# Kernel optimization log

Measured on AMD Instinct MI355X. Metric: run time of the kernel, lower is better.

The kernel has to match this reference:

```python
import jax, jax.numpy as jnp
import numpy as np

WS = (2, 7, 7)          # window size (Wd, Wh, Ww)
SS = (1, 3, 3)          # shift size
DIM = 96
HEADS = 3
HD = DIM // HEADS       # head dim = 32
N = WS[0] * WS[1] * WS[2]  # 98 tokens per window
EPS = 1e-5


def _rel_index():
    c = np.stack(np.meshgrid(np.arange(WS[0]), np.arange(WS[1]), np.arange(WS[2]), indexing='ij')).reshape(3, -1)
    r = (c[:, :, None] - c[:, None, :]).transpose(1, 2, 0)  # (N, N, 3)
    r[..., 0] += WS[0] - 1
    r[..., 1] += WS[1] - 1
    r[..., 2] += WS[2] - 1
    r[..., 0] *= (2 * WS[1] - 1) * (2 * WS[2] - 1)
    r[..., 1] *= 2 * WS[2] - 1
    return jnp.asarray(r.sum(-1))  # (N, N) int

REL_IDX = _rel_index()


def _ln(x, w, b):
    m = x.mean(-1, keepdims=True)
    v = ((x - m) ** 2).mean(-1, keepdims=True)
    return (x - m) * jax.lax.rsqrt(v + EPS) * w + b


def setup_inputs() -> dict:
    key = jax.random.key(0)
    ks = jax.random.split(key, 10)
    B, D, H, W, C = 2, 16, 112, 112, DIM
    nW = (D // WS[0]) * (H // WS[1]) * (W // WS[2])  # 2048
    s = 0.02
    tbl = (2 * WS[0] - 1) * (2 * WS[1] - 1) * (2 * WS[2] - 1)
    return dict(
        x=jax.random.normal(ks[0], (B, D, H, W, C), jnp.float32),
        mask=jax.random.normal(ks[1], (nW, N, N), jnp.float32),
        norm1_w=jnp.ones((C,), jnp.float32), norm1_b=jnp.zeros((C,), jnp.float32),
        qkv_w=jax.random.normal(ks[2], (C, 3 * C), jnp.float32) * s,
        qkv_b=jnp.zeros((3 * C,), jnp.float32),
        rpb_table=jax.random.normal(ks[3], (tbl, HEADS), jnp.float32) * s,
        proj_w=jax.random.normal(ks[4], (C, C), jnp.float32) * s,
        proj_b=jnp.zeros((C,), jnp.float32),
        norm2_w=jnp.ones((C,), jnp.float32), norm2_b=jnp.zeros((C,), jnp.float32),
        fc1_w=jax.random.normal(ks[5], (C, 4 * C), jnp.float32) * s,
        fc1_b=jnp.zeros((4 * C,), jnp.float32),
        fc2_w=jax.random.normal(ks[6], (4 * C, C), jnp.float32) * s,
        fc2_b=jnp.zeros((C,), jnp.float32),
    )


def reference(x, mask, norm1_w, norm1_b, qkv_w, qkv_b, rpb_table, proj_w, proj_b,
              norm2_w, norm2_b, fc1_w, fc1_b, fc2_w, fc2_b):
    B, D, H, W, C = x.shape
    shortcut = x
    x = _ln(x, norm1_w, norm1_b)
    # shift (dims divisible by window -> no padding needed)
    x = jnp.roll(x, shift=(-SS[0], -SS[1], -SS[2]), axis=(1, 2, 3))
    nd, nh, nw = D // WS[0], H // WS[1], W // WS[2]
    # window partition -> (B*nW, N, C)
    xw = x.reshape(B, nd, WS[0], nh, WS[1], nw, WS[2], C)
    xw = xw.transpose(0, 1, 3, 5, 2, 4, 6, 7).reshape(-1, N, C)
    B_ = xw.shape[0]
    qkv = (xw @ qkv_w + qkv_b).reshape(B_, N, 3, HEADS, HD).transpose(2, 0, 3, 1, 4)
    q, k, v = qkv[0] * (HD ** -0.5), qkv[1], qkv[2]
    attn = jnp.einsum('bhnd,bhmd->bhnm', q, k)  # (B_, H, N, N)
    bias = rpb_table[REL_IDX.reshape(-1)].reshape(N, N, HEADS).transpose(2, 0, 1)
    attn = attn + bias[None]
    nWm = mask.shape[0]
    attn = attn.reshape(B_ // nWm, nWm, HEADS, N, N) + mask[None, :, None]
    attn = jax.nn.softmax(attn.reshape(B_, HEADS, N, N), axis=-1)
    out = jnp.einsum('bhnm,bhmd->bhnd', attn, v).transpose(0, 2, 1, 3).reshape(B_, N, C)
    out = out @ proj_w + proj_b
    # window reverse
    x = out.reshape(B, nd, nh, nw, WS[0], WS[1], WS[2], C)
    x = x.transpose(0, 1, 4, 2, 5, 3, 6, 7).reshape(B, D, H, W, C)
    x = jnp.roll(x, shift=SS, axis=(1, 2, 3))
    x = shortcut + x
    y = _ln(x, norm2_w, norm2_b)
    y = jax.nn.gelu(y @ fc1_w + fc1_b, approximate=False) @ fc2_w + fc2_b
    return x + y
```

## Files before the change

kernel.cpp:

```cpp
#include <hip/hip_runtime.h>

typedef float f32x4 __attribute__((ext_vector_type(4)));
typedef __bf16 bf16x8 __attribute__((ext_vector_type(8)));
typedef unsigned short ushort_t;
typedef ushort_t us4 __attribute__((ext_vector_type(4)));
typedef ushort_t us8 __attribute__((ext_vector_type(8)));
typedef unsigned int u32x4 __attribute__((ext_vector_type(4)));

#define MFMA16(a, b, c) __builtin_amdgcn_mfma_f32_16x16x32_bf16((a), (b), (c), 0, 0, 0)

__device__ __forceinline__ ushort_t f2bf(float f) {
    unsigned int u = __builtin_bit_cast(unsigned int, f);
    u += 0x7fffu + ((u >> 16) & 1u);
    return (ushort_t)(u >> 16);
}

__device__ __forceinline__ unsigned int packbf2(float lo, float hi) {
    return ((unsigned int)f2bf(hi) << 16) | (unsigned int)f2bf(lo);
}

__device__ __forceinline__ float gelu_fast(float x) {
    float x2 = x * x;
    float t = __builtin_fmaf(0.044715f * x2, x, x);
    float e = __builtin_amdgcn_exp2f(t * (-1.5957691216f * 1.44269504f));
    return x * __builtin_amdgcn_rcpf(1.0f + e);
}

#define NTOK 98
#define CCH 96
#define QSCALE 0.17677669529663687f

#define WQKVP_OFF   ((size_t)0)
#define WPROJP_OFF  (WQKVP_OFF + (size_t)27648 * 2)
#define WFC1P_OFF   (WPROJP_OFF + (size_t)9216 * 2)
#define WFC2P_OFF   (WFC1P_OFF + (size_t)36864 * 2)
#define BIAS_OFF    (WFC2P_OFF + (size_t)36864 * 2)

__global__ __launch_bounds__(256) void prep_kernel(
    const float* __restrict__ qkv_w, const float* __restrict__ proj_w,
    const float* __restrict__ fc1_w, const float* __restrict__ fc2_w,
    const float* __restrict__ rpb,
    ushort_t* __restrict__ wqkvP, ushort_t* __restrict__ wprojP,
    ushort_t* __restrict__ wfc1P, ushort_t* __restrict__ wfc2P,
    float* __restrict__ bias)
{
    int i = blockIdx.x * 256 + threadIdx.x;
    if (i < 27648) {
        int f = i >> 9, r = i & 511, lane = r >> 3, m = r & 7;
        int k0 = f % 3, t = f / 3, nt = t % 2, t2 = t / 2, w = t2 % 3, h = t2 / 3;
        int row = k0 * 32 + (lane >> 4) * 8 + m;
        int col = w * 96 + h * 32 + nt * 16 + (lane & 15);
        wqkvP[i] = f2bf(qkv_w[row * 288 + col]);
        return;
    }
    i -= 27648;
    if (i < 9216) {
        int f = i >> 9, r = i & 511, lane = r >> 3, m = r & 7;
        int k0 = f % 3, nt = f / 3;
        int row = k0 * 32 + (lane >> 4) * 8 + m;
        int col = nt * 16 + (lane & 15);
        wprojP[i] = f2bf(proj_w[row * 96 + col]);
        return;
    }
    i -= 9216;
    if (i < 36864) {
        int f = i >> 9, r = i & 511, lane = r >> 3, m = r & 7;
        int k0 = f % 3, nt = f / 3;
        int row = k0 * 32 + (lane >> 4) * 8 + m;
        int col = nt * 16 + (lane & 15);
        wfc1P[i] = f2bf(fc1_w[row * 384 + col]);
        return;
    }
    i -= 36864;
    if (i < 36864) {
        int f = i >> 9, r = i & 511, lane = r >> 3, m = r & 7;
        int k0 = f % 12, nt = f / 12;
        int row = k0 * 32 + (lane >> 4) * 8 + m;
        int col = nt * 16 + (lane & 15);
        wfc2P[i] = f2bf(fc2_w[row * 96 + col]);
        return;
    }
    i -= 36864;
    if (i < 28812) {
        int h = i / 9604, rem = i % 9604, r = rem / 98, c = rem % 98;
        int rd = r / 49 - c / 49 + 1;
        int rh = (r % 49) / 7 - (c % 49) / 7 + 6;
        int rw = r % 7 - c % 7 + 6;
        int idx = (rd * 13 + rh) * 13 + rw;
        bias[i] = rpb[idx * 3 + h];
    }
}

__global__ __launch_bounds__(192, 3) void fused_attn(
    const float* __restrict__ x, const float* __restrict__ mask,
    const float* __restrict__ n1w, const float* __restrict__ n1b,
    const float* __restrict__ qkv_b, const float* __restrict__ proj_b,
    const ushort_t* __restrict__ wqkvP, const ushort_t* __restrict__ wprojP,
    const float* __restrict__ bias, float* __restrict__ dout)
{
    __shared__ ushort_t xw_lds[112 * 104];
    __shared__ ushort_t sc_all[3][2176];
    __shared__ int tokbase[112];

    const int tid  = threadIdx.x;
    const int lane = tid & 63;
    const int wave = tid >> 6;
    const int l16  = lane & 15, lg = lane >> 4;

    const int b  = blockIdx.x;
    const int wm = (b & 7) * 256 + ((b >> 3) >> 1);
    const int bb = (b >> 3) & 1;
    const int id_ = wm >> 8, ih = (wm >> 4) & 15, iw = wm & 15;

    if (tid < 98) {
        int td = tid / 49, r49 = tid - td * 49, th = r49 / 7, tw = r49 - th * 7;
        int od = (id_ * 2 + td + 1) & 15;
        int oh = ih * 7 + th + 3; if (oh >= 112) oh -= 112;
        int ow = iw * 7 + tw + 3; if (ow >= 112) ow -= 112;
        tokbase[tid] = ((((bb << 4) + od) * 112 + oh) * 112 + ow) * 96;
    }
    {
        us4 z4 = {0, 0, 0, 0};
        for (int i = tid; i < 14 * 26; i += 192) {
            int t = 98 + i / 26, c4 = (i % 26) * 4;
            *(us4*)(xw_lds + t * 104 + c4) = z4;
        }
    }
    __syncthreads();

    {
        const int g = tid >> 5, lane32 = tid & 31;
        for (int t = g; t < 98; t += 6) {
            const float* xp = x + tokbase[t];
            float v0 = xp[lane32], v1 = xp[lane32 + 32], v2 = xp[lane32 + 64];
            float s = v0 + v1 + v2, sq = v0 * v0 + v1 * v1 + v2 * v2;
            #pragma unroll
            for (int m = 1; m < 32; m <<= 1) { s += __shfl_xor(s, m); sq += __shfl_xor(sq, m); }
            float mean = s * (1.0f / 96.0f);
            float var = sq * (1.0f / 96.0f) - mean * mean;
            float rs = rsqrtf(var + 1e-5f);
            ushort_t* op = xw_lds + t * 104;
            op[lane32]      = f2bf((v0 - mean) * rs * n1w[lane32]      + n1b[lane32]);
            op[lane32 + 32] = f2bf((v1 - mean) * rs * n1w[lane32 + 32] + n1b[lane32 + 32]);
            op[lane32 + 64] = f2bf((v2 - mean) * rs * n1w[lane32 + 64] + n1b[lane32 + 64]);
        }
    }
    __syncthreads();

    const int h = wave;
    ushort_t* sc = sc_all[wave];
    const float* biash = bias + h * 9604;
    const float* maskw = mask + (size_t)wm * 9604;

    bf16x8 qf[7], kf[7], vf[2][4];

    #pragma unroll
    for (int which = 0; which < 2; ++which) {
        bf16x8 bw[2][3];
        float  bia[2];
        #pragma unroll
        for (int nt = 0; nt < 2; ++nt) {
            bia[nt] = qkv_b[which * 96 + h * 32 + nt * 16 + l16];
            #pragma unroll
            for (int k0 = 0; k0 < 3; ++k0)
                bw[nt][k0] = *(const bf16x8*)(wqkvP + ((((h * 3 + which) * 2 + nt) * 3 + k0) << 9) + lane * 8);
        }
        for (int mt = 0; mt < 7; ++mt) {
            const ushort_t* ap = xw_lds + (mt * 16 + l16) * 104 + lg * 8;
            bf16x8 a0 = *(const bf16x8*)(ap);
            bf16x8 a1 = *(const bf16x8*)(ap + 32);
            bf16x8 a2 = *(const bf16x8*)(ap + 64);
            #pragma unroll
            for (int nt = 0; nt < 2; ++nt) {
                f32x4 acc = {0.f, 0.f, 0.f, 0.f};
                acc = MFMA16(a0, bw[nt][0], acc);
                acc = MFMA16(a1, bw[nt][1], acc);
                acc = MFMA16(a2, bw[nt][2], acc);
                float scl = (which == 0) ? QSCALE : 1.0f;
                #pragma unroll
                for (int j = 0; j < 4; ++j)
                    sc[(lg * 4 + j) * 36 + nt * 16 + l16] = f2bf((acc[j] + bia[nt]) * scl);
            }
            if (which == 0) qf[mt] = *(const bf16x8*)(sc + l16 * 36 + lg * 8);
            else            kf[mt] = *(const bf16x8*)(sc + l16 * 36 + lg * 8);
        }
    }

    {
        bf16x8 bw[2][3];
        float  bia[2];
        #pragma unroll
        for (int nt = 0; nt < 2; ++nt) {
            bia[nt] = qkv_b[192 + h * 32 + nt * 16 + l16];
            #pragma unroll
            for (int k0 = 0; k0 < 3; ++k0)
                bw[nt][k0] = *(const bf16x8*)(wqkvP + ((((h * 3 + 2) * 2 + nt) * 3 + k0) << 9) + lane * 8);
        }
        #pragma unroll
        for (int k0 = 0; k0 < 4; ++k0) {
            unsigned int pk[2][2][2];
            #pragma unroll
            for (int half = 0; half < 2; ++half) {
                int mtp = 2 * k0 + half;
                if (mtp < 7) {
                    const ushort_t* ap = xw_lds + (mtp * 16 + l16) * 104 + lg * 8;
                    bf16x8 a0 = *(const bf16x8*)(ap);
                    bf16x8 a1 = *(const bf16x8*)(ap + 32);
                    bf16x8 a2 = *(const bf16x8*)(ap + 64);
                    #pragma unroll
                    for (int nt2 = 0; nt2 < 2; ++nt2) {
                        f32x4 acc = {0.f, 0.f, 0.f, 0.f};
                        acc = MFMA16(a0, bw[nt2][0], acc);
                        acc = MFMA16(a1, bw[nt2][1], acc);
                        acc = MFMA16(a2, bw[nt2][2], acc);
                        pk[half][nt2][0] = packbf2(acc[0] + bia[nt2], acc[1] + bia[nt2]);
                        pk[half][nt2][1] = packbf2(acc[2] + bia[nt2], acc[3] + bia[nt2]);
                    }
                } else {
                    pk[half][0][0] = pk[half][0][1] = 0u;
                    pk[half][1][0] = pk[half][1][1] = 0u;
                }
            }
            #pragma unroll
            for (int nt2 = 0; nt2 < 2; ++nt2) {
                u32x4 w;
                #pragma unroll
                for (int e = 0; e < 4; ++e) {
                    int s = l16 + 16 * (2 * (lg & 1) + (e >> 1));
                    unsigned int t0 = (unsigned int)__shfl((int)pk[0][nt2][e & 1], s, 64);
                    unsigned int t1 = (unsigned int)__shfl((int)pk[1][nt2][e & 1], s, 64);
                    w[e] = (lg >> 1) ? t1 : t0;
                }
                vf[nt2][k0] = __builtin_bit_cast(bf16x8, w);
            }
        }
    }
    __syncthreads();

    ushort_t* out = xw_lds;

    if (lane < 32) {
        us8 z = {0, 0, 0, 0, 0, 0, 0, 0};
        *(us8*)(sc + (lane >> 1) * 136 + 112 + (lane & 1) * 8) = z;
    }

    #pragma unroll
    for (int mt = 0; mt < 7; ++mt) {
        f32x4 sv[7];
        #pragma unroll
        for (int nt = 0; nt < 7; ++nt) {
            f32x4 z = {0.f, 0.f, 0.f, 0.f};
            sv[nt] = MFMA16(qf[mt], kf[nt], z);
        }
        const int r0 = mt * 16 + lg * 4;
        const bool ctail = (l16 < 2);
        #pragma unroll
        for (int j = 0; j < 4; ++j) {
            int r = r0 + j;
            if (r < 98) {
                const float* bp_ = biash + r * 98;
                const float* mp_ = maskw + r * 98;
                #pragma unroll
                for (int nt = 0; nt < 6; ++nt) {
                    int c = nt * 16 + l16;
                    sv[nt][j] += bp_[c] + mp_[c];
                }
                if (ctail) sv[6][j] += bp_[96 + l16] + mp_[96 + l16];
                else       sv[6][j] = -1e30f;
            } else {
                #pragma unroll
                for (int nt = 0; nt < 7; ++nt) sv[nt][j] = -1e30f;
            }
        }
        f32x4 inv;
        #pragma unroll
        for (int j = 0; j < 4; ++j) {
            float sum = 0.f;
            #pragma unroll
            for (int nt = 0; nt < 7; ++nt) { float e = __expf(sv[nt][j]); sv[nt][j] = e; sum += e; }
            sum += __shfl_xor(sum, 1); sum += __shfl_xor(sum, 2);
            sum += __shfl_xor(sum, 4); sum += __shfl_xor(sum, 8);
            inv[j] = __builtin_amdgcn_rcpf(sum);
        }
        #pragma unroll
        for (int j = 0; j < 4; ++j)
            #pragma unroll
            for (int nt = 0; nt < 7; ++nt)
                sc[(lg * 4 + j) * 136 + nt * 16 + l16] = f2bf(sv[nt][j]);
        bf16x8 pf[4];
        #pragma unroll
        for (int k0 = 0; k0 < 4; ++k0)
            pf[k0] = *(const bf16x8*)(sc + l16 * 136 + k0 * 32 + lg * 8);
        #pragma unroll
        for (int nt2 = 0; nt2 < 2; ++nt2) {
            f32x4 acc = {0.f, 0.f, 0.f, 0.f};
            #pragma unroll
            for (int k0 = 0; k0 < 4; ++k0) acc = MFMA16(pf[k0], vf[nt2][k0], acc);
            #pragma unroll
            for (int j = 0; j < 4; ++j) {
                int tok = mt * 16 + lg * 4 + j;
                if (tok < 98)
                    out[tok * 104 + h * 32 + nt2 * 16 + l16] = f2bf(acc[j] * inv[j]);
            }
        }
    }
    __syncthreads();

    for (int job = wave; job < 42; job += 3) {
        int mt = job / 6, nt = job % 6;
        int cg = nt * 16 + l16;
        f32x4 acc = {0.f, 0.f, 0.f, 0.f};
        #pragma unroll
        for (int k0 = 0; k0 < 3; ++k0) {
            bf16x8 ao = *(const bf16x8*)(out + (mt * 16 + l16) * 104 + k0 * 32 + lg * 8);
            bf16x8 bp = *(const bf16x8*)(wprojP + ((nt * 3 + k0) << 9) + lane * 8);
            acc = MFMA16(ao, bp, acc);
        }
        float pb = proj_b[cg];
        #pragma unroll
        for (int j = 0; j < 4; ++j) {
            int tok = mt * 16 + lg * 4 + j;
            if (tok < 98) {
                int g = tokbase[tok] + cg;
                dout[g] = x[g] + acc[j] + pb;
            }
        }
    }
}

__global__ __launch_bounds__(512, 2) void mlp_kernel(
    float* __restrict__ xres, const float* __restrict__ w2, const float* __restrict__ b2,
    const ushort_t* __restrict__ wfc1P, const float* __restrict__ fc1_b,
    const ushort_t* __restrict__ wfc2P, const float* __restrict__ fc2_b)
{
    __shared__ ushort_t A_ln[64 * 104];
    __shared__ ushort_t h_lds[64 * 392];
    const int tid = threadIdx.x;
    const int lane = tid & 63, wave = tid >> 6;
    const int l16 = lane & 15, lg = lane >> 4;
    const size_t t0 = (size_t)blockIdx.x * 64;

    {
        int t = tid >> 3, sub = tid & 7;
        const float* xp = xres + (t0 + t) * 96;
        f32x4 v[3];
        float s = 0.f, sq = 0.f;
        #pragma unroll
        for (int j4 = 0; j4 < 3; ++j4) {
            v[j4] = *(const f32x4*)(xp + (j4 * 8 + sub) * 4);
            #pragma unroll
            for (int e = 0; e < 4; ++e) { s += v[j4][e]; sq += v[j4][e] * v[j4][e]; }
        }
        s += __shfl_xor(s, 1); s += __shfl_xor(s, 2); s += __shfl_xor(s, 4);
        sq += __shfl_xor(sq, 1); sq += __shfl_xor(sq, 2); sq += __shfl_xor(sq, 4);
        float mean = s * (1.0f / 96.0f);
        float var = sq * (1.0f / 96.0f) - mean * mean;
        float rs = rsqrtf(var + 1e-5f);
        #pragma unroll
        for (int j4 = 0; j4 < 3; ++j4) {
            int c0 = (j4 * 8 + sub) * 4;
            us4 pk;
            #pragma unroll
            for (int e = 0; e < 4; ++e)
                pk[e] = f2bf((v[j4][e] - mean) * rs * w2[c0 + e] + b2[c0 + e]);
            *(us4*)(A_ln + t * 104 + c0) = pk;
        }
    }
    __syncthreads();

    for (int job = wave; job < 96; job += 8) {
        int mt = job / 24, nt = job % 24;
        int n = nt * 16 + l16;
        f32x4 acc = {0.f, 0.f, 0.f, 0.f};
        #pragma unroll
        for (int k0 = 0; k0 < 3; ++k0) {
            bf16x8 a  = *(const bf16x8*)(A_ln + (mt * 16 + l16) * 104 + k0 * 32 + lg * 8);
            bf16x8 bw = *(const bf16x8*)(wfc1P + ((nt * 3 + k0) << 9) + lane * 8);
            acc = MFMA16(a, bw, acc);
        }
        float bv = fc1_b[n];
        #pragma unroll
        for (int j = 0; j < 4; ++j) {
            int tok = mt * 16 + lg * 4 + j;
            h_lds[tok * 392 + n] = f2bf(gelu_fast(acc[j] + bv));
        }
    }
    __syncthreads();

    for (int job = wave; job < 24; job += 8) {
        int mt = job / 6, nt = job % 6;
        int c = nt * 16 + l16;
        f32x4 acc = {0.f, 0.f, 0.f, 0.f};
        #pragma unroll
        for (int k0 = 0; k0 < 12; ++k0) {
            bf16x8 a  = *(const bf16x8*)(h_lds + (mt * 16 + l16) * 392 + k0 * 32 + lg * 8);
            bf16x8 bw = *(const bf16x8*)(wfc2P + ((nt * 12 + k0) << 9) + lane * 8);
            acc = MFMA16(a, bw, acc);
        }
        float bv = fc2_b[c];
        #pragma unroll
        for (int j = 0; j < 4; ++j) {
            int tok = mt * 16 + lg * 4 + j;
            size_t g = (t0 + tok) * 96 + c;
            xres[g] = xres[g] + acc[j] + bv;
        }
    }
}

extern "C" void kernel_launch(void* const* d_in, const int* in_sizes, int n_in,
                              void* d_out, int out_size, void* d_ws, size_t ws_size,
                              hipStream_t stream) {
    const float* x      = (const float*)d_in[0];
    const float* mask   = (const float*)d_in[1];
    const float* n1w    = (const float*)d_in[2];
    const float* n1b    = (const float*)d_in[3];
    const float* qkv_w  = (const float*)d_in[4];
    const float* qkv_b  = (const float*)d_in[5];
    const float* rpb    = (const float*)d_in[6];
    const float* proj_w = (const float*)d_in[7];
    const float* proj_b = (const float*)d_in[8];
    const float* n2w    = (const float*)d_in[9];
    const float* n2b    = (const float*)d_in[10];
    const float* fc1_w  = (const float*)d_in[11];
    const float* fc1_b  = (const float*)d_in[12];
    const float* fc2_w  = (const float*)d_in[13];
    const float* fc2_b  = (const float*)d_in[14];

    char* ws = (char*)d_ws;
    ushort_t* wqkvP  = (ushort_t*)(ws + WQKVP_OFF);
    ushort_t* wprojP = (ushort_t*)(ws + WPROJP_OFF);
    ushort_t* wfc1P  = (ushort_t*)(ws + WFC1P_OFF);
    ushort_t* wfc2P  = (ushort_t*)(ws + WFC2P_OFF);
    float*    biasp  = (float*)(ws + BIAS_OFF);
    float*    dout   = (float*)d_out;

    prep_kernel<<<545, 256, 0, stream>>>(qkv_w, proj_w, fc1_w, fc2_w, rpb,
                                         wqkvP, wprojP, wfc1P, wfc2P, biasp);
    fused_attn<<<4096, 192, 0, stream>>>(x, mask, n1w, n1b, qkv_b, proj_b,
                                         wqkvP, wprojP, biasp, dout);
    mlp_kernel<<<6272, 512, 0, stream>>>(dout, n2w, n2b, wfc1P, fc1_b, wfc2P, fc2_b);
}
```

Baseline: 571.8 us.

## Transpose score tile and keep softmax in registers with bf16 mask/bias

Computes S^T (keys x queries) with MFMA so each lane's softmax reduction runs across lane groups, and builds the P operand for P·V through lane shuffles instead of an LDS round trip. The mask and relative-position bias are pre-transposed and converted to bf16 by a new pre-pass kernel, which halves their bytes read per window. The smaller LDS footprint lets occupancy rise to 4 blocks per SIMD. The cost is an extra kernel that reads the whole fp32 mask and writes a bf16 copy every call, plus a small loss of precision in the mask and bias.

```diff
diff --git a/kernel.cpp b/kernel.cpp
--- a/kernel.cpp
+++ b/kernel.cpp
@@ -4,7 +4,6 @@
 typedef __bf16 bf16x8 __attribute__((ext_vector_type(8)));
 typedef unsigned short ushort_t;
 typedef ushort_t us4 __attribute__((ext_vector_type(4)));
-typedef ushort_t us8 __attribute__((ext_vector_type(8)));
 typedef unsigned int u32x4 __attribute__((ext_vector_type(4)));
 
 #define MFMA16(a, b, c) __builtin_amdgcn_mfma_f32_16x16x32_bf16((a), (b), (c), 0, 0, 0)
@@ -14,7 +13,9 @@
     u += 0x7fffu + ((u >> 16) & 1u);
     return (ushort_t)(u >> 16);
 }
-
+__device__ __forceinline__ float bf2f(ushort_t u) {
+    return __builtin_bit_cast(float, (unsigned int)u << 16);
+}
 __device__ __forceinline__ unsigned int packbf2(float lo, float hi) {
     return ((unsigned int)f2bf(hi) << 16) | (unsigned int)f2bf(lo);
 }
@@ -34,7 +35,8 @@
 #define WPROJP_OFF  (WQKVP_OFF + (size_t)27648 * 2)
 #define WFC1P_OFF   (WPROJP_OFF + (size_t)9216 * 2)
 #define WFC2P_OFF   (WFC1P_OFF + (size_t)36864 * 2)
-#define BIAS_OFF    (WFC2P_OFF + (size_t)36864 * 2)
+#define BIAST_OFF   (WFC2P_OFF + (size_t)36864 * 2)
+#define MASKT_OFF   (BIAST_OFF + (size_t)28812 * 2 + 4096)
 
 __global__ __launch_bounds__(256) void prep_kernel(
     const float* __restrict__ qkv_w, const float* __restrict__ proj_w,
@@ -42,7 +44,7 @@
     const float* __restrict__ rpb,
     ushort_t* __restrict__ wqkvP, ushort_t* __restrict__ wprojP,
     ushort_t* __restrict__ wfc1P, ushort_t* __restrict__ wfc2P,
-    float* __restrict__ bias)
+    ushort_t* __restrict__ biasT)
 {
     int i = blockIdx.x * 256 + threadIdx.x;
     if (i < 27648) {
@@ -82,24 +84,39 @@
     }
     i -= 36864;
     if (i < 28812) {
-        int h = i / 9604, rem = i % 9604, r = rem / 98, c = rem % 98;
-        int rd = r / 49 - c / 49 + 1;
-        int rh = (r % 49) / 7 - (c % 49) / 7 + 6;
-        int rw = r % 7 - c % 7 + 6;
+        int h = i / 9604, rem = i % 9604, kc = rem / 98, qr = rem % 98;
+        int rd = qr / 49 - kc / 49 + 1;
+        int rh = (qr % 49) / 7 - (kc % 49) / 7 + 6;
+        int rw = qr % 7 - kc % 7 + 6;
         int idx = (rd * 13 + rh) * 13 + rw;
-        bias[i] = rpb[idx * 3 + h];
-    }
-}
-
-__global__ __launch_bounds__(192, 3) void fused_attn(
-    const float* __restrict__ x, const float* __restrict__ mask,
+        biasT[i] = f2bf(rpb[idx * 3 + h]);
+    }
+}
+
+__global__ __launch_bounds__(256) void maskT_kernel(
+    const float* __restrict__ mask, ushort_t* __restrict__ maskT)
+{
+    __shared__ float m_lds[9604];
+    const int wm = blockIdx.x;
+    const float* mw = mask + (size_t)wm * 9604;
+    for (int i = threadIdx.x; i < 9604; i += 256) m_lds[i] = mw[i];
+    __syncthreads();
+    ushort_t* out = maskT + (size_t)wm * 9604;
+    for (int i = threadIdx.x; i < 9604; i += 256) {
+        int kc = i / 98, qr = i - kc * 98;
+        out[i] = f2bf(m_lds[qr * 98 + kc]);
+    }
+}
+
+__global__ __launch_bounds__(192, 4) void fused_attn(
+    const float* __restrict__ x, const ushort_t* __restrict__ maskT,
     const float* __restrict__ n1w, const float* __restrict__ n1b,
     const float* __restrict__ qkv_b, const float* __restrict__ proj_b,
     const ushort_t* __restrict__ wqkvP, const ushort_t* __restrict__ wprojP,
-    const float* __restrict__ bias, float* __restrict__ dout)
+    const ushort_t* __restrict__ biasT, float* __restrict__ dout)
 {
     __shared__ ushort_t xw_lds[112 * 104];
-    __shared__ ushort_t sc_all[3][2176];
+    __shared__ ushort_t sc_all[3][576];
     __shared__ int tokbase[112];
 
     const int tid  = threadIdx.x;
@@ -149,8 +166,8 @@
 
     const int h = wave;
     ushort_t* sc = sc_all[wave];
-    const float* biash = bias + h * 9604;
-    const float* maskw = mask + (size_t)wm * 9604;
+    const ushort_t* bTh = biasT + h * 9604;
+    const ushort_t* mTw = maskT + (size_t)wm * 9604;
 
     bf16x8 qf[7], kf[7], vf[2][4];
 
@@ -198,7 +215,7 @@
         }
         #pragma unroll
         for (int k0 = 0; k0 < 4; ++k0) {
-            unsigned int pk[2][2][2];
+            unsigned int pkv[2][2][2];
             #pragma unroll
             for (int half = 0; half < 2; ++half) {
                 int mtp = 2 * k0 + half;
@@ -213,12 +230,12 @@
                         acc = MFMA16(a0, bw[nt2][0], acc);
                         acc = MFMA16(a1, bw[nt2][1], acc);
                         acc = MFMA16(a2, bw[nt2][2], acc);
-                        pk[half][nt2][0] = packbf2(acc[0] + bia[nt2], acc[1] + bia[nt2]);
-                        pk[half][nt2][1] = packbf2(acc[2] + bia[nt2], acc[3] + bia[nt2]);
+                        pkv[half][nt2][0] = packbf2(acc[0] + bia[nt2], acc[1] + bia[nt2]);
+                        pkv[half][nt2][1] = packbf2(acc[2] + bia[nt2], acc[3] + bia[nt2]);
                     }
                 } else {
-                    pk[half][0][0] = pk[half][0][1] = 0u;
-                    pk[half][1][0] = pk[half][1][1] = 0u;
+                    pkv[half][0][0] = pkv[half][0][1] = 0u;
+                    pkv[half][1][0] = pkv[half][1][1] = 0u;
                 }
             }
             #pragma unroll
@@ -227,8 +244,8 @@
                 #pragma unroll
                 for (int e = 0; e < 4; ++e) {
                     int s = l16 + 16 * (2 * (lg & 1) + (e >> 1));
-                    unsigned int t0 = (unsigned int)__shfl((int)pk[0][nt2][e & 1], s, 64);
-                    unsigned int t1 = (unsigned int)__shfl((int)pk[1][nt2][e & 1], s, 64);
+                    unsigned int t0 = (unsigned int)__shfl((int)pkv[0][nt2][e & 1], s, 64);
+                    unsigned int t1 = (unsigned int)__shfl((int)pkv[1][nt2][e & 1], s, 64);
                     w[e] = (lg >> 1) ? t1 : t0;
                 }
                 vf[nt2][k0] = __builtin_bit_cast(bf16x8, w);
@@ -239,58 +256,69 @@
 
     ushort_t* out = xw_lds;
 
-    if (lane < 32) {
-        us8 z = {0, 0, 0, 0, 0, 0, 0, 0};
-        *(us8*)(sc + (lane >> 1) * 136 + 112 + (lane & 1) * 8) = z;
-    }
-
     #pragma unroll
     for (int mt = 0; mt < 7; ++mt) {
-        f32x4 sv[7];
+        const int qr = mt * 16 + l16;
+        const ushort_t* mTl = mTw + (lg * 4) * 98 + qr;
+        const ushort_t* bTl = bTh + (lg * 4) * 98 + qr;
+
+        float sum = 0.f;
+        unsigned int pk0[7], pk1[7];
         #pragma unroll
         for (int nt = 0; nt < 7; ++nt) {
             f32x4 z = {0.f, 0.f, 0.f, 0.f};
-            sv[nt] = MFMA16(qf[mt], kf[nt], z);
-        }
-        const int r0 = mt * 16 + lg * 4;
-        const bool ctail = (l16 < 2);
-        #pragma unroll
-        for (int j = 0; j < 4; ++j) {
-            int r = r0 + j;
-            if (r < 98) {
-                const float* bp_ = biash + r * 98;
-                const float* mp_ = maskw + r * 98;
-                #pragma unroll
-                for (int nt = 0; nt < 6; ++nt) {
-                    int c = nt * 16 + l16;
-                    sv[nt][j] += bp_[c] + mp_[c];
+            f32x4 stv = MFMA16(kf[nt], qf[mt], z);
+            float e0, e1, e2, e3;
+            float ev[4];
+            #pragma unroll
+            for (int j = 0; j < 4; ++j) {
+                float val;
+                if (nt < 6) {
+                    val = stv[j] + bf2f(mTl[(nt * 16 + j) * 98]) + bf2f(bTl[(nt * 16 + j) * 98]);
+                } else {
+                    int kin = lg * 4 + j;
+                    if (kin < 2)
+                        val = stv[j] + bf2f(mTl[(96 + j) * 98]) + bf2f(bTl[(96 + j) * 98]);
+                    else
+                        val = -1e30f;
                 }
-                if (ctail) sv[6][j] += bp_[96 + l16] + mp_[96 + l16];
-                else       sv[6][j] = -1e30f;
-            } else {
-                #pragma unroll
-                for (int nt = 0; nt < 7; ++nt) sv[nt][j] = -1e30f;
-            }
-        }
-        f32x4 inv;
-        #pragma unroll
-        for (int j = 0; j < 4; ++j) {
-            float sum = 0.f;
-            #pragma unroll
-            for (int nt = 0; nt < 7; ++nt) { float e = __expf(sv[nt][j]); sv[nt][j] = e; sum += e; }
-            sum += __shfl_xor(sum, 1); sum += __shfl_xor(sum, 2);
-            sum += __shfl_xor(sum, 4); sum += __shfl_xor(sum, 8);
-            inv[j] = __builtin_amdgcn_rcpf(sum);
-        }
-        #pragma unroll
-        for (int j = 0; j < 4; ++j)
-            #pragma unroll
-            for (int nt = 0; nt < 7; ++nt)
-                sc[(lg * 4 + j) * 136 + nt * 16 + l16] = f2bf(sv[nt][j]);
+                float e_ = __expf(val);
+                sum += e_;
+                ev[j] = e_;
+            }
+            e0 = ev[0]; e1 = ev[1]; e2 = ev[2]; e3 = ev[3];
+            pk0[nt] = packbf2(e0, e1);
+            pk1[nt] = packbf2(e2, e3);
+        }
+        sum += __shfl_xor(sum, 16);
+        sum += __shfl_xor(sum, 32);
+        float inv = __builtin_amdgcn_rcpf(sum);
+
         bf16x8 pf[4];
         #pragma unroll
-        for (int k0 = 0; k0 < 4; ++k0)
-            pf[k0] = *(const bf16x8*)(sc + l16 * 136 + k0 * 32 + lg * 8);
+        for (int k0 = 0; k0 < 4; ++k0) {
+            u32x4 w;
+            #pragma unroll
+            for (int e = 0; e < 4; ++e) {
+                int s = l16 + 16 * (2 * (lg & 1) + (e >> 1));
+                unsigned int a_ = (e & 1) ? pk1[2 * k0] : pk0[2 * k0];
+                unsigned int t0 = (unsigned int)__shfl((int)a_, s, 64);
+                unsigned int t1;
+                if (k0 < 3) {
+                    unsigned int b_ = (e & 1) ? pk1[2 * k0 + 1] : pk0[2 * k0 + 1];
+                    t1 = (unsigned int)__shfl((int)b_, s, 64);
+                } else {
+                    t1 = 0u;
+                }
+                w[e] = (lg >> 1) ? t1 : t0;
+            }
+            pf[k0] = __builtin_bit_cast(bf16x8, w);
+        }
+
+        float invj[4];
+        #pragma unroll
+        for (int j = 0; j < 4; ++j) invj[j] = __shfl(inv, lg * 4 + j, 64);
+
         #pragma unroll
         for (int nt2 = 0; nt2 < 2; ++nt2) {
             f32x4 acc = {0.f, 0.f, 0.f, 0.f};
@@ -300,7 +328,7 @@
             for (int j = 0; j < 4; ++j) {
                 int tok = mt * 16 + lg * 4 + j;
                 if (tok < 98)
-                    out[tok * 104 + h * 32 + nt2 * 16 + l16] = f2bf(acc[j] * inv[j]);
+                    out[tok * 104 + h * 32 + nt2 * 16 + l16] = f2bf(acc[j] * invj[j]);
             }
         }
     }
@@ -431,12 +459,14 @@
     ushort_t* wprojP = (ushort_t*)(ws + WPROJP_OFF);
     ushort_t* wfc1P  = (ushort_t*)(ws + WFC1P_OFF);
     ushort_t* wfc2P  = (ushort_t*)(ws + WFC2P_OFF);
-    float*    biasp  = (float*)(ws + BIAS_OFF);
+    ushort_t* biasT  = (ushort_t*)(ws + BIAST_OFF);
+    ushort_t* maskT  = (ushort_t*)(ws + MASKT_OFF);
     float*    dout   = (float*)d_out;
 
     prep_kernel<<<545, 256, 0, stream>>>(qkv_w, proj_w, fc1_w, fc2_w, rpb,
-                                         wqkvP, wprojP, wfc1P, wfc2P, biasp);
-    fused_attn<<<4096, 192, 0, stream>>>(x, mask, n1w, n1b, qkv_b, proj_b,
-                                         wqkvP, wprojP, biasp, dout);
+                                         wqkvP, wprojP, wfc1P, wfc2P, biasT);
+    maskT_kernel<<<2048, 256, 0, stream>>>(mask, maskT);
+    fused_attn<<<4096, 192, 0, stream>>>(x, maskT, n1w, n1b, qkv_b, proj_b,
+                                         wqkvP, wprojP, biasT, dout);
     mlp_kernel<<<6272, 512, 0, stream>>>(dout, n2w, n2b, wfc1P, fc1_b, wfc2P, fc2_b);
 }
```

Result: slower. 667.4 us (+16.7%).

## Pre-convert mask and bias to padded bf16 MFMA layout for vectorized loads

Applied to the files above, without the earlier changes.

Adds a kernel that converts the per-window attention mask to bf16 in a tile-padded layout matching MFMA output fragments, and stores the relative position bias the same way. The attention kernel then loads mask and bias with vector loads and fuses exp and row-sum into the score loop, dropping the boundary branches. This trades scattered fp32 scalar loads for an extra conversion pass over the full mask each call and reduced mask/bias precision.

```diff
diff --git a/kernel.cpp b/kernel.cpp
--- a/kernel.cpp
+++ b/kernel.cpp
@@ -4,7 +4,6 @@
 typedef __bf16 bf16x8 __attribute__((ext_vector_type(8)));
 typedef unsigned short ushort_t;
 typedef ushort_t us4 __attribute__((ext_vector_type(4)));
-typedef ushort_t us8 __attribute__((ext_vector_type(8)));
 typedef unsigned int u32x4 __attribute__((ext_vector_type(4)));
 
 #define MFMA16(a, b, c) __builtin_amdgcn_mfma_f32_16x16x32_bf16((a), (b), (c), 0, 0, 0)
@@ -14,7 +13,9 @@
     u += 0x7fffu + ((u >> 16) & 1u);
     return (ushort_t)(u >> 16);
 }
-
+__device__ __forceinline__ float bf2f(ushort_t u) {
+    return __builtin_bit_cast(float, (unsigned int)u << 16);
+}
 __device__ __forceinline__ unsigned int packbf2(float lo, float hi) {
     return ((unsigned int)f2bf(hi) << 16) | (unsigned int)f2bf(lo);
 }
@@ -34,7 +35,8 @@
 #define WPROJP_OFF  (WQKVP_OFF + (size_t)27648 * 2)
 #define WFC1P_OFF   (WPROJP_OFF + (size_t)9216 * 2)
 #define WFC2P_OFF   (WFC1P_OFF + (size_t)36864 * 2)
-#define BIAS_OFF    (WFC2P_OFF + (size_t)36864 * 2)
+#define BIAS2_OFF   (WFC2P_OFF + (size_t)36864 * 2)
+#define MASK2_OFF   (BIAS2_OFF + (size_t)37632 * 2 + 256)
 
 __global__ __launch_bounds__(256) void prep_kernel(
     const float* __restrict__ qkv_w, const float* __restrict__ proj_w,
@@ -42,7 +44,7 @@
     const float* __restrict__ rpb,
     ushort_t* __restrict__ wqkvP, ushort_t* __restrict__ wprojP,
     ushort_t* __restrict__ wfc1P, ushort_t* __restrict__ wfc2P,
-    float* __restrict__ bias)
+    ushort_t* __restrict__ bias2)
 {
     int i = blockIdx.x * 256 + threadIdx.x;
     if (i < 27648) {
@@ -81,22 +83,49 @@
         return;
     }
     i -= 36864;
-    if (i < 28812) {
-        int h = i / 9604, rem = i % 9604, r = rem / 98, c = rem % 98;
-        int rd = r / 49 - c / 49 + 1;
-        int rh = (r % 49) / 7 - (c % 49) / 7 + 6;
-        int rw = r % 7 - c % 7 + 6;
-        int idx = (rd * 13 + rh) * 13 + rw;
-        bias[i] = rpb[idx * 3 + h];
+    if (i < 37632) {
+        int h = i / 12544, rem = i % 12544;
+        int mt = rem / 1792, rem2 = rem % 1792, kc = rem2 >> 4, r16 = rem2 & 15;
+        int row = mt * 16 + r16;
+        float v = 0.f;
+        if (row < 98 && kc < 98) {
+            int rd = row / 49 - kc / 49 + 1;
+            int rh = (row % 49) / 7 - (kc % 49) / 7 + 6;
+            int rw = row % 7 - kc % 7 + 6;
+            v = rpb[((rd * 13 + rh) * 13 + rw) * 3 + h];
+        }
+        bias2[i] = f2bf(v);
+    }
+}
+
+__global__ __launch_bounds__(256) void mask2_kernel(
+    const float* __restrict__ mask, ushort_t* __restrict__ mask2)
+{
+    __shared__ float m_lds[9604];
+    const int wm = blockIdx.x;
+    const float* mw = mask + (size_t)wm * 9604;
+    for (int i = threadIdx.x; i < 9604; i += 256) m_lds[i] = mw[i];
+    __syncthreads();
+    ushort_t* out = mask2 + (size_t)wm * 12544;
+    for (int g = threadIdx.x; g < 3136; g += 256) {
+        int mt = g / 448, rem = g % 448, kc = rem >> 2, r4 = (rem & 3) * 4;
+        us4 o;
+        #pragma unroll
+        for (int e = 0; e < 4; ++e) {
+            int row = mt * 16 + r4 + e;
+            float v = (row < 98 && kc < 98) ? m_lds[row * 98 + kc] : -1e30f;
+            o[e] = f2bf(v);
+        }
+        *(us4*)(out + (size_t)g * 4) = o;
     }
 }
 
 __global__ __launch_bounds__(192, 3) void fused_attn(
-    const float* __restrict__ x, const float* __restrict__ mask,
+    const float* __restrict__ x, const ushort_t* __restrict__ mask2,
     const float* __restrict__ n1w, const float* __restrict__ n1b,
     const float* __restrict__ qkv_b, const float* __restrict__ proj_b,
     const ushort_t* __restrict__ wqkvP, const ushort_t* __restrict__ wprojP,
-    const float* __restrict__ bias, float* __restrict__ dout)
+    const ushort_t* __restrict__ bias2, float* __restrict__ dout)
 {
     __shared__ ushort_t xw_lds[112 * 104];
     __shared__ ushort_t sc_all[3][2176];
@@ -149,8 +178,8 @@
 
     const int h = wave;
     ushort_t* sc = sc_all[wave];
-    const float* biash = bias + h * 9604;
-    const float* maskw = mask + (size_t)wm * 9604;
+    const ushort_t* m2w = mask2 + (size_t)wm * 12544;
+    const ushort_t* b2h = bias2 + (size_t)h * 12544;
 
     bf16x8 qf[7], kf[7], vf[2][4];
 
@@ -198,7 +227,7 @@
         }
         #pragma unroll
         for (int k0 = 0; k0 < 4; ++k0) {
-            unsigned int pk[2][2][2];
+            unsigned int pkv[2][2][2];
             #pragma unroll
             for (int half = 0; half < 2; ++half) {
                 int mtp = 2 * k0 + half;
@@ -213,12 +242,12 @@
                         acc = MFMA16(a0, bw[nt2][0], acc);
                         acc = MFMA16(a1, bw[nt2][1], acc);
                         acc = MFMA16(a2, bw[nt2][2], acc);
-                        pk[half][nt2][0] = packbf2(acc[0] + bia[nt2], acc[1] + bia[nt2]);
-                        pk[half][nt2][1] = packbf2(acc[2] + bia[nt2], acc[3] + bia[nt2]);
+                        pkv[half][nt2][0] = packbf2(acc[0] + bia[nt2], acc[1] + bia[nt2]);
+                        pkv[half][nt2][1] = packbf2(acc[2] + bia[nt2], acc[3] + bia[nt2]);
                     }
                 } else {
-                    pk[half][0][0] = pk[half][0][1] = 0u;
-                    pk[half][1][0] = pk[half][1][1] = 0u;
+                    pkv[half][0][0] = pkv[half][0][1] = 0u;
+                    pkv[half][1][0] = pkv[half][1][1] = 0u;
                 }
             }
             #pragma unroll
@@ -227,8 +256,8 @@
                 #pragma unroll
                 for (int e = 0; e < 4; ++e) {
                     int s = l16 + 16 * (2 * (lg & 1) + (e >> 1));
-                    unsigned int t0 = (unsigned int)__shfl((int)pk[0][nt2][e & 1], s, 64);
-                    unsigned int t1 = (unsigned int)__shfl((int)pk[1][nt2][e & 1], s, 64);
+                    unsigned int t0 = (unsigned int)__shfl((int)pkv[0][nt2][e & 1], s, 64);
+                    unsigned int t1 = (unsigned int)__shfl((int)pkv[1][nt2][e & 1], s, 64);
                     w[e] = (lg >> 1) ? t1 : t0;
                 }
                 vf[nt2][k0] = __builtin_bit_cast(bf16x8, w);
@@ -240,53 +269,41 @@
     ushort_t* out = xw_lds;
 
     if (lane < 32) {
-        us8 z = {0, 0, 0, 0, 0, 0, 0, 0};
-        *(us8*)(sc + (lane >> 1) * 136 + 112 + (lane & 1) * 8) = z;
+        us4 z4 = {0, 0, 0, 0};
+        *(us4*)(sc + (lane >> 1) * 136 + 112 + (lane & 1) * 8) = z4;
+        *(us4*)(sc + (lane >> 1) * 136 + 116 + (lane & 1) * 8) = z4;
     }
 
     #pragma unroll
     for (int mt = 0; mt < 7; ++mt) {
-        f32x4 sv[7];
+        const ushort_t* m2t = m2w + mt * 1792;
+        const ushort_t* b2t = b2h + mt * 1792;
+        us4 mv[7];
+        #pragma unroll
+        for (int nt = 0; nt < 7; ++nt)
+            mv[nt] = *(const us4*)(m2t + (nt * 16 + l16) * 16 + lg * 4);
+
+        f32x4 sums = {0.f, 0.f, 0.f, 0.f};
         #pragma unroll
         for (int nt = 0; nt < 7; ++nt) {
+            us4 bv = *(const us4*)(b2t + (nt * 16 + l16) * 16 + lg * 4);
             f32x4 z = {0.f, 0.f, 0.f, 0.f};
-            sv[nt] = MFMA16(qf[mt], kf[nt], z);
-        }
-        const int r0 = mt * 16 + lg * 4;
-        const bool ctail = (l16 < 2);
+            f32x4 stv = MFMA16(qf[mt], kf[nt], z);
+            #pragma unroll
+            for (int j = 0; j < 4; ++j) {
+                float e_ = __expf(stv[j] + bf2f(mv[nt][j]) + bf2f(bv[j]));
+                sums[j] += e_;
+                sc[(lg * 4 + j) * 136 + nt * 16 + l16] = f2bf(e_);
+            }
+        }
+        f32x4 inv;
         #pragma unroll
         for (int j = 0; j < 4; ++j) {
-            int r = r0 + j;
-            if (r < 98) {
-                const float* bp_ = biash + r * 98;
-                const float* mp_ = maskw + r * 98;
-                #pragma unroll
-                for (int nt = 0; nt < 6; ++nt) {
-                    int c = nt * 16 + l16;
-                    sv[nt][j] += bp_[c] + mp_[c];
-                }
-                if (ctail) sv[6][j] += bp_[96 + l16] + mp_[96 + l16];
-                else       sv[6][j] = -1e30f;
-            } else {
-                #pragma unroll
-                for (int nt = 0; nt < 7; ++nt) sv[nt][j] = -1e30f;
-            }
-        }
-        f32x4 inv;
-        #pragma unroll
-        for (int j = 0; j < 4; ++j) {
-            float sum = 0.f;
-            #pragma unroll
-            for (int nt = 0; nt < 7; ++nt) { float e = __expf(sv[nt][j]); sv[nt][j] = e; sum += e; }
-            sum += __shfl_xor(sum, 1); sum += __shfl_xor(sum, 2);
-            sum += __shfl_xor(sum, 4); sum += __shfl_xor(sum, 8);
-            inv[j] = __builtin_amdgcn_rcpf(sum);
-        }
-        #pragma unroll
-        for (int j = 0; j < 4; ++j)
-            #pragma unroll
-            for (int nt = 0; nt < 7; ++nt)
-                sc[(lg * 4 + j) * 136 + nt * 16 + l16] = f2bf(sv[nt][j]);
+            float s = sums[j];
+            s += __shfl_xor(s, 1); s += __shfl_xor(s, 2);
+            s += __shfl_xor(s, 4); s += __shfl_xor(s, 8);
+            inv[j] = __builtin_amdgcn_rcpf(s);
+        }
         bf16x8 pf[4];
         #pragma unroll
         for (int k0 = 0; k0 < 4; ++k0)
@@ -431,12 +448,14 @@
     ushort_t* wprojP = (ushort_t*)(ws + WPROJP_OFF);
     ushort_t* wfc1P  = (ushort_t*)(ws + WFC1P_OFF);
     ushort_t* wfc2P  = (ushort_t*)(ws + WFC2P_OFF);
-    float*    biasp  = (float*)(ws + BIAS_OFF);
+    ushort_t* bias2  = (ushort_t*)(ws + BIAS2_OFF);
+    ushort_t* mask2  = (ushort_t*)(ws + MASK2_OFF);
     float*    dout   = (float*)d_out;
 
-    prep_kernel<<<545, 256, 0, stream>>>(qkv_w, proj_w, fc1_w, fc2_w, rpb,
-                                         wqkvP, wprojP, wfc1P, wfc2P, biasp);
-    fused_attn<<<4096, 192, 0, stream>>>(x, mask, n1w, n1b, qkv_b, proj_b,
-                                         wqkvP, wprojP, biasp, dout);
+    prep_kernel<<<579, 256, 0, stream>>>(qkv_w, proj_w, fc1_w, fc2_w, rpb,
+                                         wqkvP, wprojP, wfc1P, wfc2P, bias2);
+    mask2_kernel<<<2048, 256, 0, stream>>>(mask, mask2);
+    fused_attn<<<4096, 192, 0, stream>>>(x, mask2, n1w, n1b, qkv_b, proj_b,
+                                         wqkvP, wprojP, bias2, dout);
     mlp_kernel<<<6272, 512, 0, stream>>>(dout, n2w, n2b, wfc1P, fc1_b, wfc2P, fc2_b);
 }
```

Result: faster. 504.4 us (-11.8%).
